# Kernel optimization log

Measured on AMD Instinct MI355X. Metric: run time of the kernel, lower is better.

Reference implementation:

```python
import jax, jax.numpy as jnp
import numpy as np
from jax import lax


def setup_inputs() -> dict:
    key = jax.random.key(0)
    k1, k2, k3 = jax.random.split(key, 3)
    B, K, H, W = 16, 11, 128, 128
    pred = jax.random.normal(k1, (B, K * 7, H, W), dtype=jnp.float32)
    gt = jax.random.normal(k2, (B, K, 7), dtype=jnp.float32)
    heatmap = jax.random.normal(k3, (B, K, H, W), dtype=jnp.float32)
    return {"pred": pred, "gt": gt, "heatmap": heatmap}


def reference(pred, gt, heatmap):
    B, K, H, W = heatmap.shape
    # AvgPool2d(kernel=3, stride=1, pad=1), count_include_pad=True (torch default) -> divide by 9 everywhere
    pooled = lax.reduce_window(
        heatmap, 0.0, lax.add,
        window_dimensions=(1, 1, 3, 3),
        window_strides=(1, 1, 1, 1),
        padding=((0, 0), (0, 0), (1, 1), (1, 1)),
    ) / 9.0
    # per (batch, gt-box) argmax over flattened HxW map
    index = jnp.argmax(pooled.reshape(B, K, H * W), axis=-1)  # [B, K]
    m = H  # faithful to original: x = index // m, y = index % m with m = size[2]
    x = index // m
    y = index % m
    # gather pred[b, k*7:(k+1)*7, x, y]
    predk = pred.reshape(B, K, 7, H, W)
    b_idx = jnp.arange(B)[:, None, None]          # [B,1,1]
    k_idx = jnp.arange(K)[None, :, None]          # [1,K,1]
    c_idx = jnp.arange(7)[None, None, :]          # [1,1,7]
    vals = predk[b_idx, k_idx, c_idx, x[..., None], y[..., None]]  # [B,K,7]
    diff = vals - gt[:, :, :7]
    class_loss = jnp.sum(diff * diff, axis=-1)    # MSE(reduction='sum') per (b,k)
    return class_loss.mean(axis=1)                # [B]
```

## Files before the change

### kernel.cpp

```cpp
#include <hip/hip_runtime.h>

#define HW    128
#define NPIX  16384
#define KBOX  11
#define NCH   7
#define NMAP  176
#define TILES 4
#define TROWS 32
#define NBLK  256

__global__ __launch_bounds__(NBLK) void pool_argmax_kernel(
    const float* __restrict__ heatmap,
    float* __restrict__ wsv, int* __restrict__ wsi)
{
    __shared__ float sm[(TROWS + 2) * HW];
    __shared__ float wv[NBLK / 64];
    __shared__ int   wi[NBLK / 64];

    const int bk   = blockIdx.x;
    const int tile = blockIdx.y;
    const int tid  = threadIdx.x;
    const int r0   = tile * TROWS;

    const float* base = heatmap + (size_t)bk * NPIX;

    for (int i = tid; i < ((TROWS + 2) * HW) / 4; i += NBLK) {
        const int l  = i * 4;
        const int lr = l >> 7;
        const int gr = r0 - 1 + lr;
        float4 v;
        if ((unsigned)gr < (unsigned)HW)
            v = *(const float4*)(base + ((size_t)gr << 7) + (l & 127));
        else
            v = make_float4(0.f, 0.f, 0.f, 0.f);
        *(float4*)(sm + l) = v;
    }
    __syncthreads();

    float best = -INFINITY;
    int bestIdx = 0;
    #pragma unroll
    for (int i = 0; i < (TROWS * HW) / NBLK; ++i) {
        const int p  = tid + i * NBLK;
        const int lr = p >> 7;
        const int c  = p & 127;
        float s = 0.f;
        #pragma unroll
        for (int dr = 0; dr < 3; ++dr) {
            const float* row = sm + ((lr + dr) << 7);
            s += row[c];
            if (c > 0)      s += row[c - 1];
            if (c < HW - 1) s += row[c + 1];
        }
        s *= (1.f / 9.f);
        if (s > best) { best = s; bestIdx = (r0 + lr) * HW + c; }
    }

    #pragma unroll
    for (int off = 32; off > 0; off >>= 1) {
        const float ov = __shfl_down(best, off, 64);
        const int   oi = __shfl_down(bestIdx, off, 64);
        if (ov > best || (ov == best && oi < bestIdx)) { best = ov; bestIdx = oi; }
    }
    const int wave = tid >> 6;
    if ((tid & 63) == 0) { wv[wave] = best; wi[wave] = bestIdx; }
    __syncthreads();

    if (tid == 0) {
        best = wv[0]; bestIdx = wi[0];
        #pragma unroll
        for (int w = 1; w < NBLK / 64; ++w) {
            if (wv[w] > best || (wv[w] == best && wi[w] < bestIdx)) {
                best = wv[w]; bestIdx = wi[w];
            }
        }
        wsv[bk * TILES + tile] = best;
        wsi[bk * TILES + tile] = bestIdx;
    }
}

__global__ __launch_bounds__(NBLK) void gather_loss_kernel(
    const float* __restrict__ pred, const float* __restrict__ gt,
    const float* __restrict__ wsv, const int* __restrict__ wsi,
    float* __restrict__ out)
{
    __shared__ float losses[NMAP];
    const int t = threadIdx.x;

    if (t < NMAP) {
        float best = wsv[t * TILES];
        int   bi   = wsi[t * TILES];
        #pragma unroll
        for (int s = 1; s < TILES; ++s) {
            const float v = wsv[t * TILES + s];
            const int   j = wsi[t * TILES + s];
            if (v > best || (v == best && j < bi)) { best = v; bi = j; }
        }
        const int b = t / KBOX;
        const int k = t % KBOX;
        const float* pb = pred + (size_t)(b * (KBOX * NCH) + k * NCH) * NPIX + bi;
        const float* gb = gt + (size_t)t * NCH;
        float loss = 0.f;
        #pragma unroll
        for (int c = 0; c < NCH; ++c) {
            const float d = pb[(size_t)c * NPIX] - gb[c];
            loss += d * d;
        }
        losses[t] = loss;
    }
    __syncthreads();

    if (t < NMAP / KBOX) {
        float s = 0.f;
        #pragma unroll
        for (int k = 0; k < KBOX; ++k) s += losses[t * KBOX + k];
        out[t] = s * (1.0f / KBOX);
    }
}

extern "C" void kernel_launch(void* const* d_in, const int* in_sizes, int n_in,
                              void* d_out, int out_size, void* d_ws, size_t ws_size,
                              hipStream_t stream) {
    const float* pred    = (const float*)d_in[0];
    const float* gt      = (const float*)d_in[1];
    const float* heatmap = (const float*)d_in[2];
    float* out = (float*)d_out;

    float* wsv = (float*)d_ws;
    int*   wsi = (int*)((float*)d_ws + NMAP * TILES);

    pool_argmax_kernel<<<dim3(NMAP, TILES), dim3(NBLK), 0, stream>>>(heatmap, wsv, wsi);
    gather_loss_kernel<<<dim3(1), dim3(NBLK), 0, stream>>>(pred, gt, wsv, wsi, out);
}
```

Before: 121.1 us.

## Vectorize pooling with padded LDS rows and parallelize gather per batch

The pooling tile is stored in LDS with padded 136-float rows and zero halo columns, so each thread computes four adjacent pooled outputs from float4 reads plus two neighbors, with no boundary branches. The gather kernel now launches one block per batch and one thread per (box, channel), then reduces with wave shuffles. The aim is fewer LDS instructions per output and more parallelism for the scattered pred loads. The runtime is likely dominated by streaming the heatmap from HBM, so these compute-side savings may have little effect.

New measurement: 114.9 us. 1.05x faster.

```diff
diff --git a/kernel.cpp b/kernel.cpp
--- a/kernel.cpp
+++ b/kernel.cpp
@@ -7,15 +7,16 @@
 #define NMAP  176
 #define TILES 4
 #define TROWS 32
-#define NBLK  256
+#define LROW  136
+#define LROWS 34
 
-__global__ __launch_bounds__(NBLK) void pool_argmax_kernel(
+__global__ __launch_bounds__(256) void pool_argmax_kernel(
     const float* __restrict__ heatmap,
     float* __restrict__ wsv, int* __restrict__ wsi)
 {
-    __shared__ float sm[(TROWS + 2) * HW];
-    __shared__ float wv[NBLK / 64];
-    __shared__ int   wi[NBLK / 64];
+    __shared__ float sm[LROWS * LROW];
+    __shared__ float wv[4];
+    __shared__ int   wi[4];
 
     const int bk   = blockIdx.x;
     const int tile = blockIdx.y;
@@ -24,36 +25,43 @@
 
     const float* base = heatmap + (size_t)bk * NPIX;
 
-    for (int i = tid; i < ((TROWS + 2) * HW) / 4; i += NBLK) {
-        const int l  = i * 4;
-        const int lr = l >> 7;
-        const int gr = r0 - 1 + lr;
-        float4 v;
-        if ((unsigned)gr < (unsigned)HW)
-            v = *(const float4*)(base + ((size_t)gr << 7) + (l & 127));
-        else
-            v = make_float4(0.f, 0.f, 0.f, 0.f);
-        *(float4*)(sm + l) = v;
+    for (int idx = tid; idx < LROWS * (LROW / 4); idx += 256) {
+        const int row = idx / (LROW / 4);
+        const int sc  = (idx - row * (LROW / 4)) * 4;
+        const int gr  = r0 - 1 + row;
+        float4 v = make_float4(0.f, 0.f, 0.f, 0.f);
+        if (sc >= 4 && sc <= 128 && (unsigned)gr < (unsigned)HW)
+            v = *(const float4*)(base + ((size_t)gr << 7) + (sc - 4));
+        *(float4*)(sm + row * LROW + sc) = v;
     }
     __syncthreads();
 
     float best = -INFINITY;
     int bestIdx = 0;
     #pragma unroll
-    for (int i = 0; i < (TROWS * HW) / NBLK; ++i) {
-        const int p  = tid + i * NBLK;
-        const int lr = p >> 7;
-        const int c  = p & 127;
-        float s = 0.f;
+    for (int i = 0; i < 4; ++i) {
+        const int q  = tid + i * 256;
+        const int lr = q >> 5;
+        const int c  = (q & 31) << 2;
+        float4 ps = make_float4(0.f, 0.f, 0.f, 0.f);
         #pragma unroll
         for (int dr = 0; dr < 3; ++dr) {
-            const float* row = sm + ((lr + dr) << 7);
-            s += row[c];
-            if (c > 0)      s += row[c - 1];
-            if (c < HW - 1) s += row[c + 1];
+            const float* rp = sm + (lr + dr) * LROW + 4 + c;
+            const float4 v = *(const float4*)rp;
+            const float l = rp[-1];
+            const float r = rp[4];
+            ps.x += l   + v.x + v.y;
+            ps.y += v.x + v.y + v.z;
+            ps.z += v.y + v.z + v.w;
+            ps.w += v.z + v.w + r;
         }
-        s *= (1.f / 9.f);
-        if (s > best) { best = s; bestIdx = (r0 + lr) * HW + c; }
+        ps.x *= (1.f / 9.f); ps.y *= (1.f / 9.f);
+        ps.z *= (1.f / 9.f); ps.w *= (1.f / 9.f);
+        const int pb = (r0 + lr) * HW + c;
+        if (ps.x > best) { best = ps.x; bestIdx = pb;     }
+        if (ps.y > best) { best = ps.y; bestIdx = pb + 1; }
+        if (ps.z > best) { best = ps.z; bestIdx = pb + 2; }
+        if (ps.w > best) { best = ps.w; bestIdx = pb + 3; }
     }
 
     #pragma unroll
@@ -69,7 +77,7 @@
     if (tid == 0) {
         best = wv[0]; bestIdx = wi[0];
         #pragma unroll
-        for (int w = 1; w < NBLK / 64; ++w) {
+        for (int w = 1; w < 4; ++w) {
             if (wv[w] > best || (wv[w] == best && wi[w] < bestIdx)) {
                 best = wv[w]; bestIdx = wi[w];
             }
@@ -79,43 +87,38 @@
     }
 }
 
-__global__ __launch_bounds__(NBLK) void gather_loss_kernel(
+__global__ __launch_bounds__(128) void gather_loss_kernel(
     const float* __restrict__ pred, const float* __restrict__ gt,
     const float* __restrict__ wsv, const int* __restrict__ wsi,
     float* __restrict__ out)
 {
-    __shared__ float losses[NMAP];
-    const int t = threadIdx.x;
+    __shared__ float wsum[2];
+    const int b = blockIdx.x;
+    const int j = threadIdx.x;
 
-    if (t < NMAP) {
+    float sq = 0.f;
+    if (j < KBOX * NCH) {
+        const int k = j / NCH;
+        const int c = j - k * NCH;
+        const int t = b * KBOX + k;
         float best = wsv[t * TILES];
         int   bi   = wsi[t * TILES];
         #pragma unroll
         for (int s = 1; s < TILES; ++s) {
             const float v = wsv[t * TILES + s];
-            const int   j = wsi[t * TILES + s];
-            if (v > best || (v == best && j < bi)) { best = v; bi = j; }
+            const int  ji = wsi[t * TILES + s];
+            if (v > best || (v == best && ji < bi)) { best = v; bi = ji; }
         }
-        const int b = t / KBOX;
-        const int k = t % KBOX;
-        const float* pb = pred + (size_t)(b * (KBOX * NCH) + k * NCH) * NPIX + bi;
-        const float* gb = gt + (size_t)t * NCH;
-        float loss = 0.f;
-        #pragma unroll
-        for (int c = 0; c < NCH; ++c) {
-            const float d = pb[(size_t)c * NPIX] - gb[c];
-            loss += d * d;
-        }
-        losses[t] = loss;
+        const float pv = pred[((size_t)(b * (KBOX * NCH) + k * NCH + c)) * NPIX + bi];
+        const float d  = pv - gt[(size_t)t * NCH + c];
+        sq = d * d;
     }
+
+    #pragma unroll
+    for (int off = 32; off > 0; off >>= 1) sq += __shfl_down(sq, off, 64);
+    if ((j & 63) == 0) wsum[j >> 6] = sq;
     __syncthreads();
-
-    if (t < NMAP / KBOX) {
-        float s = 0.f;
-        #pragma unroll
-        for (int k = 0; k < KBOX; ++k) s += losses[t * KBOX + k];
-        out[t] = s * (1.0f / KBOX);
-    }
+    if (j == 0) out[b] = (wsum[0] + wsum[1]) * (1.0f / KBOX);
 }
 
 extern "C" void kernel_launch(void* const* d_in, const int* in_sizes, int n_in,
@@ -129,6 +132,6 @@
     float* wsv = (float*)d_ws;
     int*   wsi = (int*)((float*)d_ws + NMAP * TILES);
 
-    pool_argmax_kernel<<<dim3(NMAP, TILES), dim3(NBLK), 0, stream>>>(heatmap, wsv, wsi);
-    gather_loss_kernel<<<dim3(1), dim3(NBLK), 0, stream>>>(pred, gt, wsv, wsi, out);
+    pool_argmax_kernel<<<dim3(NMAP, TILES), dim3(256), 0, stream>>>(heatmap, wsv, wsi);
+    gather_loss_kernel<<<dim3(16), dim3(128), 0, stream>>>(pred, gt, wsv, wsi, out);
 }
```
